# Kernel tuning notes

Measured on AMD Instinct MI355X. Metric: run time of the kernel, lower is better.

## Reference

```python
import jax, jax.numpy as jnp
import numpy as np

I, H, O = 8, 32, 1  # input_size, hidden_size, output_size


def setup_inputs() -> dict:
    key = jax.random.key(0)
    ks = jax.random.split(key, 7)
    B, T = 4096, 256
    s_ih = 1.0 / np.sqrt(H)
    inp = {
        "x": jax.random.normal(ks[0], (B, T, I), dtype=jnp.float32),
        # PyTorch nn.LSTM params, gate order [i, f, g, o]
        "W_ih": jax.random.uniform(ks[1], (4 * H, I), minval=-s_ih, maxval=s_ih, dtype=jnp.float32),
        "W_hh": jax.random.uniform(ks[2], (4 * H, H), minval=-s_ih, maxval=s_ih, dtype=jnp.float32),
        "b_ih": jax.random.uniform(ks[3], (4 * H,), minval=-s_ih, maxval=s_ih, dtype=jnp.float32),
        "b_hh": jax.random.uniform(ks[4], (4 * H,), minval=-s_ih, maxval=s_ih, dtype=jnp.float32),
        # nn.Linear(H, O)
        "W_out": jax.random.uniform(ks[5], (O, H), minval=-s_ih, maxval=s_ih, dtype=jnp.float32),
        "b_out": jax.random.uniform(ks[6], (O,), minval=-s_ih, maxval=s_ih, dtype=jnp.float32),
    }
    return inp


def _lstm_last_h(x, W_ih, W_hh, b_ih, b_hh):
    B = x.shape[0]
    # Precompute input projections for all steps: [T, B, 4H]
    x_proj = jnp.einsum("bti,gi->tbg", x, W_ih) + (b_ih + b_hh)
    h0 = jnp.zeros((B, H), dtype=x.dtype)
    c0 = jnp.zeros((B, H), dtype=x.dtype)

    def step(carry, xp):
        h, c = carry
        z = xp + h @ W_hh.T  # [B, 4H]
        i = jax.nn.sigmoid(z[:, 0 * H:1 * H])
        f = jax.nn.sigmoid(z[:, 1 * H:2 * H])
        g = jnp.tanh(z[:, 2 * H:3 * H])
        o = jax.nn.sigmoid(z[:, 3 * H:4 * H])
        c = f * c + i * g
        h = o * jnp.tanh(c)
        return (h, c), None

    (hT, _), _ = jax.lax.scan(step, (h0, c0), x_proj)
    return hT  # equals out[:, -1, :] for unidirectional batch_first LSTM


def reference(x, W_ih, W_hh, b_ih, b_hh, W_out, b_out):
    hT = _lstm_last_h(x, W_ih, W_hh, b_ih, b_hh)
    return hT @ W_out.T + b_out  # [B, O]
```

## Files before the change

kernel.cpp:

```cpp
#include <hip/hip_runtime.h>


#define T_LEN   256
#define HALF_T  128
#define XSTRIDE 130
#define LOG2E   1.4426950408889634f

typedef short bf16x8 __attribute__((ext_vector_type(8)));
typedef float f32x4  __attribute__((ext_vector_type(4)));
typedef unsigned u32x4 __attribute__((ext_vector_type(4)));

static __device__ inline short f2bf_rne(float f) {
    union { float f; unsigned u; } v; v.f = f;
    unsigned u = v.u;
    return (short)((u + 0x7FFFu + ((u >> 16) & 1u)) >> 16);
}
static __device__ inline short f2bf_fast(float f) {
    union { float f; unsigned u; } v; v.f = f;
    return (short)((v.u + 0x8000u) >> 16);
}
static __device__ inline unsigned pack_bf2(float a, float b) {
    union { float f; unsigned u; } x, y; x.f = a; y.f = b;
    return ((x.u + 0x8000u) >> 16) | ((y.u + 0x8000u) & 0xFFFF0000u);
}
static __device__ inline float bf2f(short s) {
    union { unsigned u; float f; } v;
    v.u = ((unsigned)(unsigned short)s) << 16;
    return v.f;
}

__global__ __launch_bounds__(512, 2) void lstm_kernel(
    const float* __restrict__ x, const float* __restrict__ W_ih,
    const float* __restrict__ W_hh, const float* __restrict__ b_ih,
    const float* __restrict__ b_hh, const float* __restrict__ W_out,
    const float* __restrict__ b_out, float* __restrict__ out)
{
    __shared__ __attribute__((aligned(16))) short xl[HALF_T * XSTRIDE];
    __shared__ __attribute__((aligned(16))) short h_lds[2][16 * 40];

    const int tid  = threadIdx.x;
    const int w    = tid >> 6;
    const int lane = tid & 63;
    const int L    = lane & 15;
    const int q    = lane >> 4;
    const int row0 = blockIdx.x * 16;
    const float4* xv = (const float4*)x;

    const int   n  = 32 * (L & 3) + 4 * w + (L >> 2);
    const float sc = ((L & 3) == 2 ? 2.f * LOG2E : LOG2E);
    bf16x8 whh_f, wih_f = (bf16x8){0,0,0,0,0,0,0,0};
    {
        const float* src = W_hh + n * 32 + q * 8;
#pragma unroll
        for (int j = 0; j < 8; ++j) whh_f[j] = f2bf_rne(src[j] * sc);
        if (q == 0) {
            const float* s2 = W_ih + n * 8;
#pragma unroll
            for (int j = 0; j < 8; ++j) wih_f[j] = f2bf_rne(s2[j] * sc);
        }
    }
    f32x4 bias;
#pragma unroll
    for (int r = 0; r < 4; ++r) {
        const int   nr = 32 * r + 4 * w + q;
        const float sr = (r == 2 ? 2.f * LOG2E : LOG2E);
        bias[r] = (b_ih[nr] + b_hh[nr]) * sr;
    }

    for (int i = tid; i < 16 * 40; i += 512) h_lds[0][i] = 0;

#pragma unroll
    for (int it = 0; it < 4; ++it) {
        const int idx = tid + (it << 9);
        const int L2  = idx >> 7;
        const int tl  = idx & (HALF_T - 1);
        const float4* srcp = xv + ((size_t)(row0 + L2) * T_LEN + tl) * 2;
        const float4 a = srcp[0], b = srcp[1];
        u32x4 u;
        u[0] = pack_bf2(a.x, a.y); u[1] = pack_bf2(a.z, a.w);
        u[2] = pack_bf2(b.x, b.y); u[3] = pack_bf2(b.z, b.w);
        *(u32x4*)(&xl[tl * XSTRIDE + L2 * 8]) = u;
    }
    __syncthreads();

    f32x4 zx;
    {
        const bf16x8 xf0 = *(const bf16x8*)(&xl[L * 8]);
        zx = __builtin_amdgcn_mfma_f32_16x16x32_bf16(wih_f, xf0, bias, 0, 0, 0);
    }

    float c = 0.f;
    const int hw_off = 4 * w + q;

#pragma unroll 2
    for (int t = 0; t < T_LEN; ++t) {
        if (t == HALF_T - 1) {
#pragma unroll
            for (int it = 0; it < 4; ++it) {
                const int idx = tid + (it << 9);
                const int L2  = idx >> 7;
                const int tl  = idx & (HALF_T - 1);
                const float4* srcp = xv + ((size_t)(row0 + L2) * T_LEN + HALF_T + tl) * 2;
                const float4 a = srcp[0], b = srcp[1];
                u32x4 u;
                u[0] = pack_bf2(a.x, a.y); u[1] = pack_bf2(a.z, a.w);
                u[2] = pack_bf2(b.x, b.y); u[3] = pack_bf2(b.z, b.w);
                *(u32x4*)(&xl[tl * XSTRIDE + L2 * 8]) = u;
            }
            __syncthreads();
        }

        const int par = t & 1, nxt = par ^ 1;

        const bf16x8 hfrag = *(const bf16x8*)(&h_lds[par][L * 40 + q * 8]);
        int tn = t + 1; if (tn >= T_LEN) tn = T_LEN - 1;
        const bf16x8 xfrag = *(const bf16x8*)(&xl[(tn & (HALF_T - 1)) * XSTRIDE + L * 8]);

        const f32x4 acc = __builtin_amdgcn_mfma_f32_16x16x32_bf16(whh_f, hfrag, zx, 0, 0, 0);
        zx = __builtin_amdgcn_mfma_f32_16x16x32_bf16(wih_f, xfrag, bias, 0, 0, 0);

        {
            const float ei = __builtin_amdgcn_exp2f(-acc[0]);
            const float ef = __builtin_amdgcn_exp2f(-acc[1]);
            const float eg = __builtin_amdgcn_exp2f(-acc[2]);
            const float eo = __builtin_amdgcn_exp2f(-acc[3]);
            const float fv = __builtin_amdgcn_rcpf(1.f + ef);
            const float ig = (1.f - eg) * __builtin_amdgcn_rcpf((1.f + ei) * (1.f + eg));
            c = fmaf(fv, c, ig);
            const float ec = __builtin_amdgcn_exp2f(fminf(c * (-2.f * LOG2E), 40.f));
            const float hv = (1.f - ec) * __builtin_amdgcn_rcpf((1.f + eo) * (1.f + ec));
            h_lds[nxt][L * 40 + hw_off] = f2bf_fast(hv);
        }

        __syncthreads();
    }

    if (tid < 16) {
        float s = b_out[0];
#pragma unroll
        for (int k = 0; k < 32; ++k) s = fmaf(bf2f(h_lds[0][tid * 40 + k]), W_out[k], s);
        out[row0 + tid] = s;
    }
}

extern "C" void kernel_launch(void* const* d_in, const int* in_sizes, int n_in,
                              void* d_out, int out_size, void* d_ws, size_t ws_size,
                              hipStream_t stream) {
    const float* x     = (const float*)d_in[0];
    const float* W_ih  = (const float*)d_in[1];
    const float* W_hh  = (const float*)d_in[2];
    const float* b_ih  = (const float*)d_in[3];
    const float* b_hh  = (const float*)d_in[4];
    const float* W_out = (const float*)d_in[5];
    const float* b_out = (const float*)d_in[6];
    float* out = (float*)d_out;

    const int B = in_sizes[0] / (T_LEN * 8);
    const int tiles = B / 16;
    lstm_kernel<<<tiles, 512, 0, stream>>>(x, W_ih, W_hh, b_ih, b_hh, W_out, b_out, out);
}
```

Measured before the change: 140.3 us.

## Halve waves per block with two hidden units per lane and XOR-swizzled x tile

Each block now runs 4 waves instead of 8, and each lane computes two hidden units with two MFMAs per step. This halves the barrier participants and the number of waves per recurrent step. The x staging buffer drops its padded stride in favour of an XOR swizzle, and h is written as packed pairs. The final output projection now uses the fp32 h with shuffles instead of reading bf16 h back from LDS. In exchange each wave has a longer serial dependency chain per step, and the new launch bounds target one block per SIMD group.

```diff
diff --git a/kernel.cpp b/kernel.cpp
--- a/kernel.cpp
+++ b/kernel.cpp
@@ -3,7 +3,6 @@
 
 #define T_LEN   256
 #define HALF_T  128
-#define XSTRIDE 130
 #define LOG2E   1.4426950408889634f
 
 typedef short bf16x8 __attribute__((ext_vector_type(8)));
@@ -15,63 +14,56 @@
     unsigned u = v.u;
     return (short)((u + 0x7FFFu + ((u >> 16) & 1u)) >> 16);
 }
-static __device__ inline short f2bf_fast(float f) {
-    union { float f; unsigned u; } v; v.f = f;
-    return (short)((v.u + 0x8000u) >> 16);
-}
 static __device__ inline unsigned pack_bf2(float a, float b) {
     union { float f; unsigned u; } x, y; x.f = a; y.f = b;
     return ((x.u + 0x8000u) >> 16) | ((y.u + 0x8000u) & 0xFFFF0000u);
 }
-static __device__ inline float bf2f(short s) {
-    union { unsigned u; float f; } v;
-    v.u = ((unsigned)(unsigned short)s) << 16;
-    return v.f;
-}
 
-__global__ __launch_bounds__(512, 2) void lstm_kernel(
+__global__ __launch_bounds__(256, 1) void lstm_kernel(
     const float* __restrict__ x, const float* __restrict__ W_ih,
     const float* __restrict__ W_hh, const float* __restrict__ b_ih,
     const float* __restrict__ b_hh, const float* __restrict__ W_out,
     const float* __restrict__ b_out, float* __restrict__ out)
 {
-    __shared__ __attribute__((aligned(16))) short xl[HALF_T * XSTRIDE];
+    __shared__ __attribute__((aligned(16))) short xl[HALF_T * 128];
     __shared__ __attribute__((aligned(16))) short h_lds[2][16 * 40];
 
     const int tid  = threadIdx.x;
-    const int w    = tid >> 6;
+    const int s    = tid >> 6;
     const int lane = tid & 63;
     const int L    = lane & 15;
     const int q    = lane >> 4;
     const int row0 = blockIdx.x * 16;
     const float4* xv = (const float4*)x;
 
-    const int   n  = 32 * (L & 3) + 4 * w + (L >> 2);
-    const float sc = ((L & 3) == 2 ? 2.f * LOG2E : LOG2E);
-    bf16x8 whh_f, wih_f = (bf16x8){0,0,0,0,0,0,0,0};
-    {
+    bf16x8 whh[2], wih[2];
+    f32x4  bias[2];
+    const float scL = ((L & 3) == 2 ? 2.f * LOG2E : LOG2E);
+#pragma unroll
+    for (int m = 0; m < 2; ++m) {
+        const int n = 32 * (L & 3) + 8 * s + 2 * (L >> 2) + m;
         const float* src = W_hh + n * 32 + q * 8;
 #pragma unroll
-        for (int j = 0; j < 8; ++j) whh_f[j] = f2bf_rne(src[j] * sc);
+        for (int j = 0; j < 8; ++j) whh[m][j] = f2bf_rne(src[j] * scL);
+        wih[m] = (bf16x8){0,0,0,0,0,0,0,0};
         if (q == 0) {
             const float* s2 = W_ih + n * 8;
 #pragma unroll
-            for (int j = 0; j < 8; ++j) wih_f[j] = f2bf_rne(s2[j] * sc);
+            for (int j = 0; j < 8; ++j) wih[m][j] = f2bf_rne(s2[j] * scL);
+        }
+#pragma unroll
+        for (int r = 0; r < 4; ++r) {
+            const int   nr = 32 * r + 8 * s + 2 * q + m;
+            const float sr = (r == 2 ? 2.f * LOG2E : LOG2E);
+            bias[m][r] = (b_ih[nr] + b_hh[nr]) * sr;
         }
     }
-    f32x4 bias;
-#pragma unroll
-    for (int r = 0; r < 4; ++r) {
-        const int   nr = 32 * r + 4 * w + q;
-        const float sr = (r == 2 ? 2.f * LOG2E : LOG2E);
-        bias[r] = (b_ih[nr] + b_hh[nr]) * sr;
-    }
-
-    for (int i = tid; i < 16 * 40; i += 512) h_lds[0][i] = 0;
+    const int   hoff = 8 * s + 2 * q;
+    const float Wo0 = W_out[hoff], Wo1 = W_out[hoff + 1];
 
 #pragma unroll
-    for (int it = 0; it < 4; ++it) {
-        const int idx = tid + (it << 9);
+    for (int k = 0; k < 8; ++k) {
+        const int idx = tid + (k << 8);
         const int L2  = idx >> 7;
         const int tl  = idx & (HALF_T - 1);
         const float4* srcp = xv + ((size_t)(row0 + L2) * T_LEN + tl) * 2;
@@ -79,25 +71,26 @@
         u32x4 u;
         u[0] = pack_bf2(a.x, a.y); u[1] = pack_bf2(a.z, a.w);
         u[2] = pack_bf2(b.x, b.y); u[3] = pack_bf2(b.z, b.w);
-        *(u32x4*)(&xl[tl * XSTRIDE + L2 * 8]) = u;
+        *(u32x4*)(&xl[tl * 128 + ((L2 ^ (tl & 7)) << 3)]) = u;
     }
     __syncthreads();
 
-    f32x4 zx;
+    f32x4 zx0, zx1;
     {
         const bf16x8 xf0 = *(const bf16x8*)(&xl[L * 8]);
-        zx = __builtin_amdgcn_mfma_f32_16x16x32_bf16(wih_f, xf0, bias, 0, 0, 0);
+        zx0 = __builtin_amdgcn_mfma_f32_16x16x32_bf16(wih[0], xf0, bias[0], 0, 0, 0);
+        zx1 = __builtin_amdgcn_mfma_f32_16x16x32_bf16(wih[1], xf0, bias[1], 0, 0, 0);
     }
 
-    float c = 0.f;
-    const int hw_off = 4 * w + q;
+    bf16x8 hfrag = (bf16x8){0,0,0,0,0,0,0,0};
+    float c0 = 0.f, c1 = 0.f, h0v = 0.f, h1v = 0.f;
 
 #pragma unroll 2
     for (int t = 0; t < T_LEN; ++t) {
         if (t == HALF_T - 1) {
 #pragma unroll
-            for (int it = 0; it < 4; ++it) {
-                const int idx = tid + (it << 9);
+            for (int k = 0; k < 8; ++k) {
+                const int idx = tid + (k << 8);
                 const int L2  = idx >> 7;
                 const int tl  = idx & (HALF_T - 1);
                 const float4* srcp = xv + ((size_t)(row0 + L2) * T_LEN + HALF_T + tl) * 2;
@@ -105,42 +98,60 @@
                 u32x4 u;
                 u[0] = pack_bf2(a.x, a.y); u[1] = pack_bf2(a.z, a.w);
                 u[2] = pack_bf2(b.x, b.y); u[3] = pack_bf2(b.z, b.w);
-                *(u32x4*)(&xl[tl * XSTRIDE + L2 * 8]) = u;
+                *(u32x4*)(&xl[tl * 128 + ((L2 ^ (tl & 7)) << 3)]) = u;
             }
             __syncthreads();
         }
 
-        const int par = t & 1, nxt = par ^ 1;
+        const f32x4 a0 = __builtin_amdgcn_mfma_f32_16x16x32_bf16(whh[0], hfrag, zx0, 0, 0, 0);
+        const f32x4 a1 = __builtin_amdgcn_mfma_f32_16x16x32_bf16(whh[1], hfrag, zx1, 0, 0, 0);
 
-        const bf16x8 hfrag = *(const bf16x8*)(&h_lds[par][L * 40 + q * 8]);
         int tn = t + 1; if (tn >= T_LEN) tn = T_LEN - 1;
-        const bf16x8 xfrag = *(const bf16x8*)(&xl[(tn & (HALF_T - 1)) * XSTRIDE + L * 8]);
-
-        const f32x4 acc = __builtin_amdgcn_mfma_f32_16x16x32_bf16(whh_f, hfrag, zx, 0, 0, 0);
-        zx = __builtin_amdgcn_mfma_f32_16x16x32_bf16(wih_f, xfrag, bias, 0, 0, 0);
+        const bf16x8 xfrag = *(const bf16x8*)(
+            &xl[(tn & (HALF_T - 1)) * 128 + ((L ^ (tn & 7)) << 3)]);
+        zx0 = __builtin_amdgcn_mfma_f32_16x16x32_bf16(wih[0], xfrag, bias[0], 0, 0, 0);
+        zx1 = __builtin_amdgcn_mfma_f32_16x16x32_bf16(wih[1], xfrag, bias[1], 0, 0, 0);
 
         {
-            const float ei = __builtin_amdgcn_exp2f(-acc[0]);
-            const float ef = __builtin_amdgcn_exp2f(-acc[1]);
-            const float eg = __builtin_amdgcn_exp2f(-acc[2]);
-            const float eo = __builtin_amdgcn_exp2f(-acc[3]);
+            const float ei = __builtin_amdgcn_exp2f(-a0[0]);
+            const float ef = __builtin_amdgcn_exp2f(-a0[1]);
+            const float eg = __builtin_amdgcn_exp2f(-a0[2]);
+            const float eo = __builtin_amdgcn_exp2f(-a0[3]);
             const float fv = __builtin_amdgcn_rcpf(1.f + ef);
             const float ig = (1.f - eg) * __builtin_amdgcn_rcpf((1.f + ei) * (1.f + eg));
-            c = fmaf(fv, c, ig);
-            const float ec = __builtin_amdgcn_exp2f(fminf(c * (-2.f * LOG2E), 40.f));
-            const float hv = (1.f - ec) * __builtin_amdgcn_rcpf((1.f + eo) * (1.f + ec));
-            h_lds[nxt][L * 40 + hw_off] = f2bf_fast(hv);
+            c0 = fmaf(fv, c0, ig);
+            const float ec = __builtin_amdgcn_exp2f(fminf(c0 * (-2.f * LOG2E), 40.f));
+            h0v = (1.f - ec) * __builtin_amdgcn_rcpf((1.f + eo) * (1.f + ec));
+        }
+        {
+            const float ei = __builtin_amdgcn_exp2f(-a1[0]);
+            const float ef = __builtin_amdgcn_exp2f(-a1[1]);
+            const float eg = __builtin_amdgcn_exp2f(-a1[2]);
+            const float eo = __builtin_amdgcn_exp2f(-a1[3]);
+            const float fv = __builtin_amdgcn_rcpf(1.f + ef);
+            const float ig = (1.f - eg) * __builtin_amdgcn_rcpf((1.f + ei) * (1.f + eg));
+            c1 = fmaf(fv, c1, ig);
+            const float ec = __builtin_amdgcn_exp2f(fminf(c1 * (-2.f * LOG2E), 40.f));
+            h1v = (1.f - ec) * __builtin_amdgcn_rcpf((1.f + eo) * (1.f + ec));
         }
 
-        __syncthreads();
+        if (t != T_LEN - 1) {
+            const int nxt = (t & 1) ^ 1;
+            *(unsigned*)(&h_lds[nxt][L * 40 + hoff]) = pack_bf2(h0v, h1v);
+            __syncthreads();
+            hfrag = *(const bf16x8*)(&h_lds[nxt][L * 40 + 8 * q]);
+        }
     }
 
-    if (tid < 16) {
-        float s = b_out[0];
-#pragma unroll
-        for (int k = 0; k < 32; ++k) s = fmaf(bf2f(h_lds[0][tid * 40 + k]), W_out[k], s);
-        out[row0 + tid] = s;
-    }
+    float partial = fmaf(h0v, Wo0, h1v * Wo1);
+    partial += __shfl_xor(partial, 16, 64);
+    partial += __shfl_xor(partial, 32, 64);
+    float* po = (float*)h_lds;
+    if (lane < 16) po[s * 16 + lane] = partial;
+    __syncthreads();
+    if (tid < 16)
+        out[row0 + tid] = po[tid] + po[16 + tid] + po[32 + tid] + po[48 + tid]
+                        + b_out[0];
 }
 
 extern "C" void kernel_launch(void* const* d_in, const int* in_sizes, int n_in,
@@ -157,5 +168,5 @@
 
     const int B = in_sizes[0] / (T_LEN * 8);
     const int tiles = B / 16;
-    lstm_kernel<<<tiles, 512, 0, stream>>>(x, W_ih, W_hh, b_ih, b_hh, W_out, b_out, out);
+    lstm_kernel<<<tiles, 256, 0, stream>>>(x, W_ih, W_hh, b_ih, b_hh, W_out, b_out, out);
 }
```

Measured after the change: 150.8 us. 1.07x slower.

## Stream x directly from global into registers with a two-step prefetch

Applied to the files above, without the earlier changes.

Drops the LDS staging buffer for x and its mid-sequence refill barrier. Each lane now loads its row's next-but-one timestep straight from global memory into registers and packs it to bf16 right before the input-projection MFMA. The per-step __syncthreads is replaced by an explicit lgkmcnt wait plus s_barrier, so outstanding global loads are not drained at every step. This cuts LDS traffic and footprint, but adds a global-latency dependency every step, and all 8 waves redundantly load the same x data.

```diff
diff --git a/kernel.cpp b/kernel.cpp
--- a/kernel.cpp
+++ b/kernel.cpp
@@ -2,8 +2,6 @@
 
 
 #define T_LEN   256
-#define HALF_T  128
-#define XSTRIDE 130
 #define LOG2E   1.4426950408889634f
 
 typedef short bf16x8 __attribute__((ext_vector_type(8)));
@@ -35,7 +33,6 @@
     const float* __restrict__ b_hh, const float* __restrict__ W_out,
     const float* __restrict__ b_out, float* __restrict__ out)
 {
-    __shared__ __attribute__((aligned(16))) short xl[HALF_T * XSTRIDE];
     __shared__ __attribute__((aligned(16))) short h_lds[2][16 * 40];
 
     const int tid  = threadIdx.x;
@@ -44,7 +41,6 @@
     const int L    = lane & 15;
     const int q    = lane >> 4;
     const int row0 = blockIdx.x * 16;
-    const float4* xv = (const float4*)x;
 
     const int   n  = 32 * (L & 3) + 4 * w + (L >> 2);
     const float sc = ((L & 3) == 2 ? 2.f * LOG2E : LOG2E);
@@ -69,55 +65,42 @@
 
     for (int i = tid; i < 16 * 40; i += 512) h_lds[0][i] = 0;
 
-#pragma unroll
-    for (int it = 0; it < 4; ++it) {
-        const int idx = tid + (it << 9);
-        const int L2  = idx >> 7;
-        const int tl  = idx & (HALF_T - 1);
-        const float4* srcp = xv + ((size_t)(row0 + L2) * T_LEN + tl) * 2;
-        const float4 a = srcp[0], b = srcp[1];
-        u32x4 u;
-        u[0] = pack_bf2(a.x, a.y); u[1] = pack_bf2(a.z, a.w);
-        u[2] = pack_bf2(b.x, b.y); u[3] = pack_bf2(b.z, b.w);
-        *(u32x4*)(&xl[tl * XSTRIDE + L2 * 8]) = u;
-    }
+    const float4* xbase = (const float4*)x + (size_t)(row0 + L) * (T_LEN * 2);
+    float4 ra = xbase[0], rb = xbase[1];
+
     __syncthreads();
 
     f32x4 zx;
     {
-        const bf16x8 xf0 = *(const bf16x8*)(&xl[L * 8]);
+        u32x4 u;
+        u[0] = pack_bf2(ra.x, ra.y); u[1] = pack_bf2(ra.z, ra.w);
+        u[2] = pack_bf2(rb.x, rb.y); u[3] = pack_bf2(rb.z, rb.w);
+        const bf16x8 xf0 = *(const bf16x8*)&u;
         zx = __builtin_amdgcn_mfma_f32_16x16x32_bf16(wih_f, xf0, bias, 0, 0, 0);
     }
+    ra = xbase[2]; rb = xbase[3];
 
     float c = 0.f;
     const int hw_off = 4 * w + q;
 
 #pragma unroll 2
     for (int t = 0; t < T_LEN; ++t) {
-        if (t == HALF_T - 1) {
-#pragma unroll
-            for (int it = 0; it < 4; ++it) {
-                const int idx = tid + (it << 9);
-                const int L2  = idx >> 7;
-                const int tl  = idx & (HALF_T - 1);
-                const float4* srcp = xv + ((size_t)(row0 + L2) * T_LEN + HALF_T + tl) * 2;
-                const float4 a = srcp[0], b = srcp[1];
-                u32x4 u;
-                u[0] = pack_bf2(a.x, a.y); u[1] = pack_bf2(a.z, a.w);
-                u[2] = pack_bf2(b.x, b.y); u[3] = pack_bf2(b.z, b.w);
-                *(u32x4*)(&xl[tl * XSTRIDE + L2 * 8]) = u;
-            }
-            __syncthreads();
-        }
-
         const int par = t & 1, nxt = par ^ 1;
 
         const bf16x8 hfrag = *(const bf16x8*)(&h_lds[par][L * 40 + q * 8]);
-        int tn = t + 1; if (tn >= T_LEN) tn = T_LEN - 1;
-        const bf16x8 xfrag = *(const bf16x8*)(&xl[(tn & (HALF_T - 1)) * XSTRIDE + L * 8]);
+
+        bf16x8 xfn;
+        {
+            u32x4 u;
+            u[0] = pack_bf2(ra.x, ra.y); u[1] = pack_bf2(ra.z, ra.w);
+            u[2] = pack_bf2(rb.x, rb.y); u[3] = pack_bf2(rb.z, rb.w);
+            xfn = *(const bf16x8*)&u;
+        }
+        int tn2 = t + 2; if (tn2 > T_LEN - 1) tn2 = T_LEN - 1;
+        ra = xbase[2 * tn2]; rb = xbase[2 * tn2 + 1];
 
         const f32x4 acc = __builtin_amdgcn_mfma_f32_16x16x32_bf16(whh_f, hfrag, zx, 0, 0, 0);
-        zx = __builtin_amdgcn_mfma_f32_16x16x32_bf16(wih_f, xfrag, bias, 0, 0, 0);
+        zx = __builtin_amdgcn_mfma_f32_16x16x32_bf16(wih_f, xfn, bias, 0, 0, 0);
 
         {
             const float ei = __builtin_amdgcn_exp2f(-acc[0]);
@@ -132,7 +115,9 @@
             h_lds[nxt][L * 40 + hw_off] = f2bf_fast(hv);
         }
 
-        __syncthreads();
+        asm volatile("s_waitcnt lgkmcnt(0)" ::: "memory");
+        __builtin_amdgcn_s_barrier();
+        asm volatile("" ::: "memory");
     }
 
     if (tid < 16) {
```

Measured after the change: 189.9 us. +35.3%, slower.
